# Kernel optimization log

Measured on AMD Instinct MI355X. Metric: run time of the kernel, lower is better.

The kernel has to match this reference:

```python
import jax, jax.numpy as jnp
import numpy as np

N = 50000   # nodes
E = 800000  # edges (before self loops)
D = 128     # n_embd
H = 4       # heads
C = D // H  # per-head channels
NEG_SLOPE = 0.2
EPS = 1e-5


def _ln(x, w):
    m = jnp.mean(x, axis=-1, keepdims=True)
    v = jnp.mean((x - m) ** 2, axis=-1, keepdims=True)
    return (x - m) / jnp.sqrt(v + EPS) * w


def setup_inputs() -> dict:
    key = jax.random.key(0)
    ks = jax.random.split(key, 8)
    s = 0.02
    return {
        "x": jax.random.normal(ks[0], (N, D), jnp.float32),
        "edge_index": jax.random.randint(ks[1], (2, E), 0, N, jnp.int32),
        "ln1_w": jnp.ones((D,), jnp.float32),
        "Wl": jax.random.normal(ks[2], (D, D), jnp.float32) * s,
        "bl": jnp.zeros((D,), jnp.float32),
        "Wr": jax.random.normal(ks[3], (D, D), jnp.float32) * s,
        "br": jnp.zeros((D,), jnp.float32),
        "att": jax.random.normal(ks[4], (H, C), jnp.float32) * s,
        "gat_bias": jnp.zeros((D,), jnp.float32),
        "ln2_w": jnp.ones((D,), jnp.float32),
        "W_fc": jax.random.normal(ks[5], (D, 4 * D), jnp.float32) * s,
        "W_proj": jax.random.normal(ks[6], (4 * D, D), jnp.float32) * s,
    }


def reference(x, edge_index, ln1_w, Wl, bl, Wr, br, att, gat_bias, ln2_w, W_fc, W_proj):
    n = x.shape[0]
    # add self loops (GATv2Conv default)
    loops = jnp.arange(n, dtype=edge_index.dtype)
    src = jnp.concatenate([edge_index[0], loops])  # message sources (x_j)
    dst = jnp.concatenate([edge_index[1], loops])  # message targets (x_i)

    h = _ln(x, ln1_w)
    xl = (h @ Wl + bl).reshape(n, H, C)  # source transform
    xr = (h @ Wr + br).reshape(n, H, C)  # target transform

    # GATv2 edge-wise attention
    e = jax.nn.leaky_relu(xl[src] + xr[dst], NEG_SLOPE)      # [E+N, H, C]
    score = jnp.einsum('ehc,hc->eh', e, att)                  # [E+N, H]
    smax = jax.ops.segment_max(score, dst, num_segments=n)    # [N, H]
    ex = jnp.exp(score - smax[dst])
    denom = jax.ops.segment_sum(ex, dst, num_segments=n)      # [N, H]
    alpha = ex / denom[dst]                                   # segment softmax
    agg = jax.ops.segment_sum(alpha[:, :, None] * xl[src], dst, num_segments=n)

    x = x + agg.reshape(n, H * C) + gat_bias

    h2 = _ln(x, ln2_w)
    x = x + jax.nn.gelu(h2 @ W_fc, approximate=False) @ W_proj
    return x
```

## Files before the change

### kernel.cpp

```cpp
#include <hip/hip_runtime.h>
#include <math.h>

typedef __attribute__((ext_vector_type(8))) short bf16x8;
typedef __attribute__((ext_vector_type(4))) float f32x4;

__device__ __forceinline__ unsigned bf16b(float f) {
  unsigned u = __float_as_uint(f);
  return (u + 0x7fffu + ((u >> 16) & 1u)) >> 16;
}
__device__ __forceinline__ unsigned packbf(float lo, float hi) {
  return bf16b(lo) | (bf16b(hi) << 16);
}
__device__ __forceinline__ float unpk_lo(unsigned u) { return __uint_as_float(u << 16); }
__device__ __forceinline__ float unpk_hi(unsigned u) { return __uint_as_float(u & 0xffff0000u); }
__device__ __forceinline__ float gelu_f(float v) {
  return 0.5f * v * (1.0f + erff(v * 0.70710678118654752f));
}

__global__ void k_cvtz(const float* __restrict__ Wl, const float* __restrict__ Wr,
                       const float* __restrict__ Wfc, const float* __restrict__ Wpj,
                       unsigned short* __restrict__ Wl_t, unsigned short* __restrict__ Wr_t,
                       unsigned short* __restrict__ Wfc_t, unsigned short* __restrict__ Wpj_t,
                       int* __restrict__ deg, int* __restrict__ cursor, int n) {
  int i = blockIdx.x * 256 + threadIdx.x;
  if (i < n) { deg[i] = 0; cursor[i] = 0; }
  if (i < 16384) {
    int k = i & 127, c = i >> 7;
    Wl_t[i] = (unsigned short)bf16b(Wl[k * 128 + c]);
    Wr_t[i] = (unsigned short)bf16b(Wr[k * 128 + c]);
  } else if (i < 81920) {
    int j = i - 16384;
    int k = j & 127, c = j >> 7;
    Wfc_t[j] = (unsigned short)bf16b(Wfc[(size_t)k * 512 + c]);
  } else if (i < 147456) {
    int j = i - 81920;
    int k = j & 511, c = j >> 9;
    Wpj_t[j] = (unsigned short)bf16b(Wpj[(size_t)k * 128 + c]);
  }
}

__global__ __launch_bounds__(256, 2) void k_gemlr(
    const float* __restrict__ x, const float* __restrict__ ln1w,
    const unsigned short* __restrict__ Wl_t, const float* __restrict__ bl,
    const unsigned short* __restrict__ Wr_t, const float* __restrict__ br,
    unsigned short* __restrict__ xl16, unsigned short* __restrict__ xr16, int n)
{
  __shared__ __align__(16) unsigned short hs[64 * 128];
  const int t = threadIdx.x;
  const int lane = t & 63, w = t >> 6;
  const int r0 = blockIdx.x * 64;

  {
    const int row = t >> 2, seg = t & 3;
    const int gr = r0 + row;
    const float4* xr4 = (const float4*)(x + (size_t)(gr < n ? gr : 0) * 128) + seg * 8;
    float4 v[8];
    #pragma unroll
    for (int j = 0; j < 8; ++j) v[j] = (gr < n) ? xr4[j] : make_float4(0.f,0.f,0.f,0.f);
    float s = 0.f;
    #pragma unroll
    for (int j = 0; j < 8; ++j) s += v[j].x + v[j].y + v[j].z + v[j].w;
    s += __shfl_xor(s, 1); s += __shfl_xor(s, 2);
    const float mean = s * (1.0f / 128.0f);
    float vv = 0.f;
    #pragma unroll
    for (int j = 0; j < 8; ++j) {
      float a = v[j].x - mean, b = v[j].y - mean, c = v[j].z - mean, d = v[j].w - mean;
      vv += a * a + b * b + c * c + d * d;
    }
    vv += __shfl_xor(vv, 1); vv += __shfl_xor(vv, 2);
    const float rstd = rsqrtf(vv * (1.0f / 128.0f) + 1e-5f);
    #pragma unroll
    for (int j2 = 0; j2 < 4; ++j2) {
      float4 wa = ((const float4*)ln1w)[seg * 8 + 2 * j2];
      float4 wb = ((const float4*)ln1w)[seg * 8 + 2 * j2 + 1];
      const float4 va = v[2 * j2], vb = v[2 * j2 + 1];
      uint4 pk;
      pk.x = packbf((va.x - mean) * rstd * wa.x, (va.y - mean) * rstd * wa.y);
      pk.y = packbf((va.z - mean) * rstd * wa.z, (va.w - mean) * rstd * wa.w);
      pk.z = packbf((vb.x - mean) * rstd * wb.x, (vb.y - mean) * rstd * wb.y);
      pk.w = packbf((vb.z - mean) * rstd * wb.z, (vb.w - mean) * rstd * wb.w);
      int byteoff = (row * 256 + (seg * 4 + j2) * 16) ^ ((row & 7) << 4);
      *(uint4*)((char*)hs + byteoff) = pk;
    }
  }
  __syncthreads();

  const int l15 = lane & 15, lg = lane >> 4;
  const unsigned short* __restrict__ Wt = (w < 2) ? Wl_t : Wr_t;
  const float* __restrict__ bias = (w < 2) ? bl : br;
  unsigned short* __restrict__ outp = (w < 2) ? xl16 : xr16;
  const int cbase = (w & 1) * 64;

  f32x4 acc[4][4];
  #pragma unroll
  for (int m = 0; m < 4; ++m)
    #pragma unroll
    for (int nf = 0; nf < 4; ++nf) acc[m][nf] = (f32x4){0.f, 0.f, 0.f, 0.f};

  #pragma unroll
  for (int ks = 0; ks < 4; ++ks) {
    bf16x8 b[4];
    #pragma unroll
    for (int nf = 0; nf < 4; ++nf) {
      const int c = cbase + nf * 16 + l15;
      b[nf] = *(const bf16x8*)(Wt + (size_t)c * 128 + ks * 32 + lg * 8);
    }
    bf16x8 a[4];
    #pragma unroll
    for (int m = 0; m < 4; ++m) {
      const int row = m * 16 + l15;
      const int byteoff = (row * 256 + ks * 64 + lg * 16) ^ ((row & 7) << 4);
      a[m] = *(const bf16x8*)((const char*)hs + byteoff);
    }
    #pragma unroll
    for (int m = 0; m < 4; ++m)
      #pragma unroll
      for (int nf = 0; nf < 4; ++nf)
        acc[m][nf] = __builtin_amdgcn_mfma_f32_16x16x32_bf16(a[m], b[nf], acc[m][nf], 0, 0, 0);
  }

  #pragma unroll
  for (int nf = 0; nf < 4; ++nf) {
    const int c = cbase + nf * 16 + l15;
    const float bv = bias[c];
    #pragma unroll
    for (int m = 0; m < 4; ++m) {
      #pragma unroll
      for (int r = 0; r < 4; ++r) {
        const int gr = r0 + m * 16 + lg * 4 + r;
        if (gr < n)
          outp[(size_t)gr * 128 + c] = (unsigned short)bf16b(acc[m][nf][r] + bv);
      }
    }
  }
}

__global__ void k_hist(const int* __restrict__ dst, int* __restrict__ deg, int E) {
  int e = blockIdx.x * 256 + threadIdx.x;
  if (e < E) atomicAdd(&deg[dst[e]], 1);
}

__global__ void k_scan1(const int* __restrict__ deg, int* __restrict__ bsum, int n) {
  __shared__ int red[4];
  const int t = threadIdx.x, lane = t & 63, w = t >> 6;
  const int i = blockIdx.x * 256 + t;
  int v = (i < n) ? deg[i] : 0;
  #pragma unroll
  for (int off = 1; off < 64; off <<= 1) v += __shfl_xor(v, off);
  if (lane == 0) red[w] = v;
  __syncthreads();
  if (t == 0) bsum[blockIdx.x] = red[0] + red[1] + red[2] + red[3];
}

__global__ void k_scan2(int* __restrict__ bsum, int nb, int* __restrict__ rowptr,
                        int n, int Etot) {
  __shared__ int wsum[16];
  const int t = threadIdx.x, lane = t & 63, w = t >> 6;
  const int v = (t < nb) ? bsum[t] : 0;
  int incl = v;
  #pragma unroll
  for (int off = 1; off < 64; off <<= 1) {
    int u = __shfl_up(incl, off);
    if (lane >= off) incl += u;
  }
  if (lane == 63) wsum[w] = incl;
  __syncthreads();
  if (w == 0 && lane < 16) {
    int sv = wsum[lane];
    int si = sv;
    #pragma unroll
    for (int off = 1; off < 16; off <<= 1) {
      int u = __shfl_up(si, off);
      if (lane >= off) si += u;
    }
    wsum[lane] = si - sv;
  }
  __syncthreads();
  if (t < nb) bsum[t] = wsum[w] + incl - v;
  if (t == 0) rowptr[n] = Etot;
}

__global__ void k_scan3(const int* __restrict__ deg, const int* __restrict__ bsum,
                        int* __restrict__ rowptr, int n) {
  __shared__ int ws4[4];
  const int t = threadIdx.x, lane = t & 63, w = t >> 6;
  const int i = blockIdx.x * 256 + t;
  const int v = (i < n) ? deg[i] : 0;
  int incl = v;
  #pragma unroll
  for (int off = 1; off < 64; off <<= 1) {
    int u = __shfl_up(incl, off);
    if (lane >= off) incl += u;
  }
  if (lane == 63) ws4[w] = incl;
  __syncthreads();
  if (t == 0) {
    int s1 = ws4[0], s2 = s1 + ws4[1], s3 = s2 + ws4[2];
    ws4[0] = 0; ws4[1] = s1; ws4[2] = s2; ws4[3] = s3;
  }
  __syncthreads();
  if (i < n) rowptr[i] = bsum[blockIdx.x] + ws4[w] + incl - v;
}

__global__ void k_scatter(const int* __restrict__ src, const int* __restrict__ dst,
                          const int* __restrict__ rowptr, int* __restrict__ cursor,
                          int* __restrict__ csr, int E) {
  int e = blockIdx.x * 256 + threadIdx.x;
  if (e < E) {
    int d = dst[e];
    int pos = atomicAdd(&cursor[d], 1);
    csr[rowptr[d] + pos] = src[e];
  }
}

__global__ __launch_bounds__(256) void k_attn(
    const float* __restrict__ x, const unsigned* __restrict__ xlp,
    const unsigned* __restrict__ xrp, const float* __restrict__ att,
    const float* __restrict__ gbias, const float* __restrict__ ln2w,
    const int* __restrict__ rowptr, const int* __restrict__ csr,
    float* __restrict__ x2, unsigned* __restrict__ h2p, int n)
{
  const int d = (int)((blockIdx.x * blockDim.x + threadIdx.x) >> 6);
  if (d >= n) return;
  const int l = threadIdx.x & 63;
  const unsigned xr = xrp[(size_t)d * 64 + l];
  const float xr0 = unpk_lo(xr), xr1 = unpk_hi(xr);
  const float2 at = ((const float2*)att)[l];
  const int beg = rowptr[d], end = rowptr[d + 1];
  const int cnt = end - beg;

  float m, s, acc0, acc1;
  {
    const unsigned xs = xlp[(size_t)d * 64 + l];
    const float a0 = unpk_lo(xs), a1 = unpk_hi(xs);
    float e0 = a0 + xr0; e0 = (e0 > 0.f) ? e0 : 0.2f * e0;
    float e1 = a1 + xr1; e1 = (e1 > 0.f) ? e1 : 0.2f * e1;
    float tt = e0 * at.x + e1 * at.y;
    tt += __shfl_xor(tt, 1); tt += __shfl_xor(tt, 2);
    tt += __shfl_xor(tt, 4); tt += __shfl_xor(tt, 8);
    m = tt; s = 1.f; acc0 = a0; acc1 = a1;
  }

  unsigned pxs[4];
  if (cnt > 0) {
    int idx[4];
    #pragma unroll
    for (int i = 0; i < 4; ++i) idx[i] = (i < cnt) ? csr[beg + i] : d;
    #pragma unroll
    for (int i = 0; i < 4; ++i) pxs[i] = xlp[(size_t)idx[i] * 64 + l];
  }
  for (int b = 0; b < cnt; b += 4) {
    unsigned xs[4];
    #pragma unroll
    for (int i = 0; i < 4; ++i) xs[i] = pxs[i];
    if (b + 4 < cnt) {
      int idx[4];
      #pragma unroll
      for (int i = 0; i < 4; ++i) idx[i] = (b + 4 + i < cnt) ? csr[beg + b + 4 + i] : d;
      #pragma unroll
      for (int i = 0; i < 4; ++i) pxs[i] = xlp[(size_t)idx[i] * 64 + l];
    }
    const int rem = cnt - b;
    float A0[4], A1[4], T[4];
    #pragma unroll
    for (int i = 0; i < 4; ++i) {
      A0[i] = unpk_lo(xs[i]); A1[i] = unpk_hi(xs[i]);
      float e0 = A0[i] + xr0; e0 = (e0 > 0.f) ? e0 : 0.2f * e0;
      float e1 = A1[i] + xr1; e1 = (e1 > 0.f) ? e1 : 0.2f * e1;
      T[i] = e0 * at.x + e1 * at.y;
    }
    #pragma unroll
    for (int off = 1; off < 16; off <<= 1)
      #pragma unroll
      for (int i = 0; i < 4; ++i) T[i] += __shfl_xor(T[i], off);
    #pragma unroll
    for (int i = 0; i < 4; ++i) if (i >= rem) T[i] = -1e30f;
    const float bm = fmaxf(fmaxf(T[0], T[1]), fmaxf(T[2], T[3]));
    const float p0 = __expf(T[0] - bm), p1 = __expf(T[1] - bm);
    const float p2 = __expf(T[2] - bm), p3 = __expf(T[3] - bm);
    const float bs = p0 + p1 + p2 + p3;
    const float b0 = p0 * A0[0] + p1 * A0[1] + p2 * A0[2] + p3 * A0[3];
    const float b1 = p0 * A1[0] + p1 * A1[1] + p2 * A1[2] + p3 * A1[3];
    const float nm = fmaxf(m, bm);
    const float sc = __expf(m - nm), sb = __expf(bm - nm);
    s    = s    * sc + bs * sb;
    acc0 = acc0 * sc + b0 * sb;
    acc1 = acc1 * sc + b1 * sb;
    m = nm;
  }

  const float inv = 1.0f / s;
  const float2 xv = ((const float2*)x)[(size_t)d * 64 + l];
  const float2 gb = ((const float2*)gbias)[l];
  float2 o;
  o.x = xv.x + acc0 * inv + gb.x;
  o.y = xv.y + acc1 * inv + gb.y;
  ((float2*)x2)[(size_t)d * 64 + l] = o;

  float s2 = o.x + o.y;
  #pragma unroll
  for (int off = 1; off < 64; off <<= 1) s2 += __shfl_xor(s2, off);
  const float mean = s2 * (1.0f / 128.0f);
  const float dx = o.x - mean, dy = o.y - mean;
  float vv = dx * dx + dy * dy;
  #pragma unroll
  for (int off = 1; off < 64; off <<= 1) vv += __shfl_xor(vv, off);
  const float rstd = rsqrtf(vv * (1.0f / 128.0f) + 1e-5f);
  const float2 lw = ((const float2*)ln2w)[l];
  h2p[(size_t)d * 64 + l] = packbf(dx * rstd * lw.x, dy * rstd * lw.y);
}

__global__ __launch_bounds__(256, 3) void k_fc(
    const unsigned short* __restrict__ h2, const unsigned short* __restrict__ Wfc_t,
    unsigned short* __restrict__ g, int n)
{
  __shared__ __align__(16) unsigned short As[128 * 128];
  __shared__ __align__(16) unsigned short Bs[64 * 128];
  const int t = threadIdx.x, lane = t & 63, w = t >> 6;
  const int l15 = lane & 15, lg = lane >> 4;
  const int r0 = blockIdx.x * 128;
  const int cb0 = blockIdx.y * 64;

  #pragma unroll
  for (int it = 0; it < 8; ++it) {
    int i = it * 256 + t;
    int row = i >> 4, c16 = i & 15;
    int gr = r0 + row;
    uint4 v = make_uint4(0, 0, 0, 0);
    if (gr < n) v = *(const uint4*)(h2 + (size_t)gr * 128 + c16 * 8);
    *(uint4*)((char*)As + ((row * 256 + c16 * 16) ^ ((row & 7) << 4))) = v;
  }
  #pragma unroll
  for (int it = 0; it < 4; ++it) {
    int i = it * 256 + t;
    int col = i >> 4, k16 = i & 15;
    uint4 v = *(const uint4*)(Wfc_t + (size_t)(cb0 + col) * 128 + k16 * 8);
    *(uint4*)((char*)Bs + ((col * 256 + k16 * 16) ^ ((col & 7) << 4))) = v;
  }
  __syncthreads();

  const int rbase = (w >> 1) * 64;
  const int cbase = (w & 1) * 32;
  f32x4 acc[4][2];
  #pragma unroll
  for (int m = 0; m < 4; ++m) {
    acc[m][0] = (f32x4){0.f, 0.f, 0.f, 0.f};
    acc[m][1] = (f32x4){0.f, 0.f, 0.f, 0.f};
  }
  #pragma unroll
  for (int ks = 0; ks < 4; ++ks) {
    bf16x8 b[2], a[4];
    #pragma unroll
    for (int nf = 0; nf < 2; ++nf) {
      const int col = cbase + nf * 16 + l15;
      b[nf] = *(const bf16x8*)((const char*)Bs + ((col * 256 + ks * 64 + lg * 16) ^ ((col & 7) << 4)));
    }
    #pragma unroll
    for (int m = 0; m < 4; ++m) {
      const int row = rbase + m * 16 + l15;
      a[m] = *(const bf16x8*)((const char*)As + ((row * 256 + ks * 64 + lg * 16) ^ ((row & 7) << 4)));
    }
    #pragma unroll
    for (int m = 0; m < 4; ++m) {
      acc[m][0] = __builtin_amdgcn_mfma_f32_16x16x32_bf16(a[m], b[0], acc[m][0], 0, 0, 0);
      acc[m][1] = __builtin_amdgcn_mfma_f32_16x16x32_bf16(a[m], b[1], acc[m][1], 0, 0, 0);
    }
  }

  #pragma unroll
  for (int m = 0; m < 4; ++m)
    #pragma unroll
    for (int nf = 0; nf < 2; ++nf) {
      const int gc = cb0 + cbase + nf * 16 + l15;
      #pragma unroll
      for (int r = 0; r < 4; ++r) {
        const int gr = r0 + rbase + m * 16 + lg * 4 + r;
        if (gr < n)
          g[(size_t)gr * 256 + gc] = (unsigned short)bf16b(gelu_f(acc[m][nf][r]));
      }
    }
}

__global__ __launch_bounds__(256, 3) void k_proj(
    const unsigned short* __restrict__ g, const unsigned short* __restrict__ Wpj_t,
    float* __restrict__ out, int n)
{
  __shared__ __align__(16) unsigned short As[64 * 64];
  __shared__ __align__(16) unsigned short Bs[128 * 64];
  const int t = threadIdx.x, lane = t & 63, w = t >> 6;
  const int l15 = lane & 15, lg = lane >> 4;
  const int r0 = blockIdx.x * 64;

  f32x4 acc[8];
  #pragma unroll
  for (int nf = 0; nf < 8; ++nf) acc[nf] = (f32x4){0.f, 0.f, 0.f, 0.f};

  for (int kt = 0; kt < 4; ++kt) {
    __syncthreads();
    #pragma unroll
    for (int it = 0; it < 2; ++it) {
      int i = it * 256 + t;
      int row = i >> 3, k8 = i & 7;
      int gr = r0 + row;
      uint4 v = make_uint4(0, 0, 0, 0);
      if (gr < n) v = *(const uint4*)(g + (size_t)gr * 256 + kt * 64 + k8 * 8);
      *(uint4*)((char*)As + ((row * 128 + k8 * 16) ^ ((row & 7) << 4))) = v;
    }
    #pragma unroll
    for (int it = 0; it < 4; ++it) {
      int i = it * 256 + t;
      int col = i >> 3, k8 = i & 7;
      uint4 v = *(const uint4*)(Wpj_t + (size_t)col * 512 + kt * 64 + k8 * 8);
      *(uint4*)((char*)Bs + ((col * 128 + k8 * 16) ^ ((col & 7) << 4))) = v;
    }
    __syncthreads();

    #pragma unroll
    for (int ks = 0; ks < 2; ++ks) {
      const int row = w * 16 + l15;
      bf16x8 a = *(const bf16x8*)((const char*)As + ((row * 128 + ks * 64 + lg * 16) ^ ((row & 7) << 4)));
      bf16x8 b[8];
      #pragma unroll
      for (int nf = 0; nf < 8; ++nf) {
        const int col = nf * 16 + l15;
        b[nf] = *(const bf16x8*)((const char*)Bs + ((col * 128 + ks * 64 + lg * 16) ^ ((col & 7) << 4)));
      }
      #pragma unroll
      for (int nf = 0; nf < 8; ++nf)
        acc[nf] = __builtin_amdgcn_mfma_f32_16x16x32_bf16(a, b[nf], acc[nf], 0, 0, 0);
    }
  }

  #pragma unroll
  for (int nf = 0; nf < 8; ++nf) {
    const int col = nf * 16 + l15;
    #pragma unroll
    for (int r = 0; r < 4; ++r) {
      const int gr = r0 + w * 16 + lg * 4 + r;
      if (gr < n) {
        float* p = out + (size_t)gr * 128 + col;
        *p = *p + acc[nf][r];
      }
    }
  }
}

extern "C" void kernel_launch(void* const* d_in, const int* in_sizes, int n_in,
                              void* d_out, int out_size, void* d_ws, size_t ws_size,
                              hipStream_t stream)
{
  (void)n_in; (void)out_size; (void)ws_size;
  const float* x     = (const float*)d_in[0];
  const int*   ei    = (const int*)d_in[1];
  const float* ln1w  = (const float*)d_in[2];
  const float* Wl    = (const float*)d_in[3];
  const float* bl    = (const float*)d_in[4];
  const float* Wr    = (const float*)d_in[5];
  const float* br    = (const float*)d_in[6];
  const float* att   = (const float*)d_in[7];
  const float* gbias = (const float*)d_in[8];
  const float* ln2w  = (const float*)d_in[9];
  const float* Wfc   = (const float*)d_in[10];
  const float* Wpj   = (const float*)d_in[11];
  float* out = (float*)d_out;

  const int n = in_sizes[0] / 128;
  const int E = in_sizes[1] / 2;
  const int nb = (n + 255) / 256;

  char* w = (char*)d_ws;
  unsigned short* h2    = (unsigned short*)w; w += (size_t)n * 128 * 2;
  unsigned short* Wl_t  = (unsigned short*)w; w += 16384 * 2;
  unsigned short* Wr_t  = (unsigned short*)w; w += 16384 * 2;
  unsigned short* Wfc_t = (unsigned short*)w; w += 65536 * 2;
  unsigned short* Wpj_t = (unsigned short*)w; w += 65536 * 2;
  int* rowptr = (int*)w; w += (size_t)((n + 4) & ~3) * 4;
  int* bsum   = (int*)w; w += 1024 * 4;
  int* deg    = (int*)w; w += (size_t)n * 4;
  int* cursor = (int*)w; w += (size_t)n * 4;
  char* gbase = w;
  unsigned short* xl16 = (unsigned short*)gbase;
  unsigned short* xr16 = (unsigned short*)(gbase + (size_t)n * 128 * 2);
  int* csr             = (int*)(gbase + (size_t)n * 128 * 4);
  unsigned short* g    = (unsigned short*)gbase;

  k_cvtz<<<576, 256, 0, stream>>>(Wl, Wr, Wfc, Wpj, Wl_t, Wr_t, Wfc_t, Wpj_t,
                                  deg, cursor, n);
  k_gemlr<<<(n + 63) / 64, 256, 0, stream>>>(x, ln1w, Wl_t, bl, Wr_t, br, xl16, xr16, n);
  k_hist<<<(E + 255) / 256, 256, 0, stream>>>(ei + E, deg, E);
  k_scan1<<<nb, 256, 0, stream>>>(deg, bsum, n);
  k_scan2<<<1, 1024, 0, stream>>>(bsum, nb, rowptr, n, E);
  k_scan3<<<nb, 256, 0, stream>>>(deg, bsum, rowptr, n);
  k_scatter<<<(E + 255) / 256, 256, 0, stream>>>(ei, ei + E, rowptr, cursor, csr, E);
  k_attn<<<(n + 3) / 4, 256, 0, stream>>>(x, (const unsigned*)xl16, (const unsigned*)xr16,
                                          att, gbias, ln2w, rowptr, csr, out,
                                          (unsigned*)h2, n);
  dim3 gfc((n + 127) / 128, 4);
  for (int half = 0; half < 2; ++half) {
    k_fc  <<<gfc, 256, 0, stream>>>(h2, Wfc_t + (size_t)half * 256 * 128, g, n);
    k_proj<<<(n + 63) / 64, 256, 0, stream>>>(g, Wpj_t + (size_t)half * 256, out, n);
  }
}
```

Baseline: 379.7 us.

## Retile MLP, merge fc/proj halves, widen attention gather, tile weight transpose

Several changes land together. The MLP now runs as a single fc pass over all 512 hidden columns and one proj pass with K=512 when the workspace is large enough, with the fc tile reshaped to 64 rows by 128 columns; this removes the second pair of launches and the two read-modify-write passes over the output. The attention gather prefetches 8 neighbours per batch instead of 4 and makes the indices wave-uniform via readfirstlane, aiming for more memory-level parallelism. The weight-conversion kernel now transposes through a shared-memory tile with vectorised reads and writes instead of strided per-element reads. The costs are higher register pressure in attention and a larger workspace footprint for the intermediate g buffer.

```diff
diff --git a/kernel.cpp b/kernel.cpp
--- a/kernel.cpp
+++ b/kernel.cpp
@@ -21,21 +21,42 @@
                        const float* __restrict__ Wfc, const float* __restrict__ Wpj,
                        unsigned short* __restrict__ Wl_t, unsigned short* __restrict__ Wr_t,
                        unsigned short* __restrict__ Wfc_t, unsigned short* __restrict__ Wpj_t,
-                       int* __restrict__ deg, int* __restrict__ cursor, int n) {
-  int i = blockIdx.x * 256 + threadIdx.x;
-  if (i < n) { deg[i] = 0; cursor[i] = 0; }
-  if (i < 16384) {
-    int k = i & 127, c = i >> 7;
-    Wl_t[i] = (unsigned short)bf16b(Wl[k * 128 + c]);
-    Wr_t[i] = (unsigned short)bf16b(Wr[k * 128 + c]);
-  } else if (i < 81920) {
-    int j = i - 16384;
-    int k = j & 127, c = j >> 7;
-    Wfc_t[j] = (unsigned short)bf16b(Wfc[(size_t)k * 512 + c]);
-  } else if (i < 147456) {
-    int j = i - 81920;
-    int k = j & 511, c = j >> 9;
-    Wpj_t[j] = (unsigned short)bf16b(Wpj[(size_t)k * 128 + c]);
+                       int* __restrict__ deg, int* __restrict__ cursor, int n, int nzb) {
+  __shared__ float tl[64 * 65];
+  const int b = blockIdx.x, t = threadIdx.x;
+  if (b >= 40) {
+    const int zb = b - 40;
+    int* arr = (zb < nzb) ? deg : cursor;
+    const int base = (zb % nzb) * 1024 + t * 4;
+    #pragma unroll
+    for (int j = 0; j < 4; ++j) if (base + j < n) arr[base + j] = 0;
+    return;
+  }
+  const float* src; unsigned short* dst; int K, C, tm;
+  if (b < 4)       { src = Wl;  dst = Wl_t;  K = 128; C = 128; tm = b; }
+  else if (b < 8)  { src = Wr;  dst = Wr_t;  K = 128; C = 128; tm = b - 4; }
+  else if (b < 24) { src = Wfc; dst = Wfc_t; K = 128; C = 512; tm = b - 8; }
+  else             { src = Wpj; dst = Wpj_t; K = 512; C = 128; tm = b - 24; }
+  const int ct = C >> 6;
+  const int k0 = (tm / ct) * 64, c0 = (tm % ct) * 64;
+  #pragma unroll
+  for (int it = 0; it < 4; ++it) {
+    const int q = it * 256 + t;
+    const int row = q >> 4, c4 = q & 15;
+    float4 v = *(const float4*)(src + (size_t)(k0 + row) * C + c0 + c4 * 4);
+    float* p = &tl[row * 65 + c4 * 4];
+    p[0] = v.x; p[1] = v.y; p[2] = v.z; p[3] = v.w;
+  }
+  __syncthreads();
+  #pragma unroll
+  for (int it = 0; it < 2; ++it) {
+    const int q = it * 256 + t;
+    const int cr = q >> 3, k8 = q & 7;
+    bf16x8 sh;
+    #pragma unroll
+    for (int j = 0; j < 8; ++j)
+      sh[j] = (short)bf16b(tl[(k8 * 8 + j) * 65 + cr]);
+    *(bf16x8*)(dst + (size_t)(c0 + cr) * K + k0 + k8 * 8) = sh;
   }
 }
 
@@ -221,10 +242,11 @@
     const int* __restrict__ rowptr, const int* __restrict__ csr,
     float* __restrict__ x2, unsigned* __restrict__ h2p, int n)
 {
-  const int d = (int)((blockIdx.x * blockDim.x + threadIdx.x) >> 6);
-  if (d >= n) return;
+  const int dv = (int)((blockIdx.x * blockDim.x + threadIdx.x) >> 6);
+  if (dv >= n) return;
+  const int d = __builtin_amdgcn_readfirstlane(dv);
   const int l = threadIdx.x & 63;
-  const unsigned xr = xrp[(size_t)d * 64 + l];
+  const unsigned xr = (xrp + (size_t)d * 64)[l];
   const float xr0 = unpk_lo(xr), xr1 = unpk_hi(xr);
   const float2 at = ((const float2*)att)[l];
   const int beg = rowptr[d], end = rowptr[d + 1];
@@ -232,56 +254,62 @@
 
   float m, s, acc0, acc1;
   {
-    const unsigned xs = xlp[(size_t)d * 64 + l];
+    const unsigned xs = (xlp + (size_t)d * 64)[l];
     const float a0 = unpk_lo(xs), a1 = unpk_hi(xs);
-    float e0 = a0 + xr0; e0 = (e0 > 0.f) ? e0 : 0.2f * e0;
-    float e1 = a1 + xr1; e1 = (e1 > 0.f) ? e1 : 0.2f * e1;
+    const float t0 = a0 + xr0, t1 = a1 + xr1;
+    const float e0 = fmaxf(t0, 0.2f * t0), e1 = fmaxf(t1, 0.2f * t1);
     float tt = e0 * at.x + e1 * at.y;
     tt += __shfl_xor(tt, 1); tt += __shfl_xor(tt, 2);
     tt += __shfl_xor(tt, 4); tt += __shfl_xor(tt, 8);
     m = tt; s = 1.f; acc0 = a0; acc1 = a1;
   }
 
-  unsigned pxs[4];
+  unsigned pxs[8];
   if (cnt > 0) {
-    int idx[4];
-    #pragma unroll
-    for (int i = 0; i < 4; ++i) idx[i] = (i < cnt) ? csr[beg + i] : d;
-    #pragma unroll
-    for (int i = 0; i < 4; ++i) pxs[i] = xlp[(size_t)idx[i] * 64 + l];
-  }
-  for (int b = 0; b < cnt; b += 4) {
-    unsigned xs[4];
-    #pragma unroll
-    for (int i = 0; i < 4; ++i) xs[i] = pxs[i];
-    if (b + 4 < cnt) {
-      int idx[4];
-      #pragma unroll
-      for (int i = 0; i < 4; ++i) idx[i] = (b + 4 + i < cnt) ? csr[beg + b + 4 + i] : d;
-      #pragma unroll
-      for (int i = 0; i < 4; ++i) pxs[i] = xlp[(size_t)idx[i] * 64 + l];
+    #pragma unroll
+    for (int i = 0; i < 8; ++i) {
+      int idx = (i < cnt) ? csr[beg + i] : d;
+      idx = __builtin_amdgcn_readfirstlane(idx);
+      pxs[i] = (xlp + (size_t)idx * 64)[l];
+    }
+  }
+  for (int b = 0; b < cnt; b += 8) {
+    unsigned xs[8];
+    #pragma unroll
+    for (int i = 0; i < 8; ++i) xs[i] = pxs[i];
+    if (b + 8 < cnt) {
+      #pragma unroll
+      for (int i = 0; i < 8; ++i) {
+        int idx = (b + 8 + i < cnt) ? csr[beg + b + 8 + i] : d;
+        idx = __builtin_amdgcn_readfirstlane(idx);
+        pxs[i] = (xlp + (size_t)idx * 64)[l];
+      }
     }
     const int rem = cnt - b;
-    float A0[4], A1[4], T[4];
-    #pragma unroll
-    for (int i = 0; i < 4; ++i) {
+    float A0[8], A1[8], T[8];
+    #pragma unroll
+    for (int i = 0; i < 8; ++i) {
       A0[i] = unpk_lo(xs[i]); A1[i] = unpk_hi(xs[i]);
-      float e0 = A0[i] + xr0; e0 = (e0 > 0.f) ? e0 : 0.2f * e0;
-      float e1 = A1[i] + xr1; e1 = (e1 > 0.f) ? e1 : 0.2f * e1;
+      const float t0 = A0[i] + xr0, t1 = A1[i] + xr1;
+      const float e0 = fmaxf(t0, 0.2f * t0), e1 = fmaxf(t1, 0.2f * t1);
       T[i] = e0 * at.x + e1 * at.y;
     }
     #pragma unroll
     for (int off = 1; off < 16; off <<= 1)
       #pragma unroll
-      for (int i = 0; i < 4; ++i) T[i] += __shfl_xor(T[i], off);
-    #pragma unroll
-    for (int i = 0; i < 4; ++i) if (i >= rem) T[i] = -1e30f;
-    const float bm = fmaxf(fmaxf(T[0], T[1]), fmaxf(T[2], T[3]));
-    const float p0 = __expf(T[0] - bm), p1 = __expf(T[1] - bm);
-    const float p2 = __expf(T[2] - bm), p3 = __expf(T[3] - bm);
-    const float bs = p0 + p1 + p2 + p3;
-    const float b0 = p0 * A0[0] + p1 * A0[1] + p2 * A0[2] + p3 * A0[3];
-    const float b1 = p0 * A1[0] + p1 * A1[1] + p2 * A1[2] + p3 * A1[3];
+      for (int i = 0; i < 8; ++i) T[i] += __shfl_xor(T[i], off);
+    #pragma unroll
+    for (int i = 0; i < 8; ++i) if (i >= rem) T[i] = -1e30f;
+    float bm = fmaxf(fmaxf(fmaxf(T[0], T[1]), fmaxf(T[2], T[3])),
+                     fmaxf(fmaxf(T[4], T[5]), fmaxf(T[6], T[7])));
+    float P[8], bs = 0.f, b0 = 0.f, b1 = 0.f;
+    #pragma unroll
+    for (int i = 0; i < 8; ++i) {
+      P[i] = __expf(T[i] - bm);
+      bs += P[i];
+      b0 += P[i] * A0[i];
+      b1 += P[i] * A1[i];
+    }
     const float nm = fmaxf(m, bm);
     const float sc = __expf(m - nm), sb = __expf(bm - nm);
     s    = s    * sc + bs * sb;
@@ -291,12 +319,12 @@
   }
 
   const float inv = 1.0f / s;
-  const float2 xv = ((const float2*)x)[(size_t)d * 64 + l];
+  const float2 xv = ((const float2*)(x + (size_t)d * 128))[l];
   const float2 gb = ((const float2*)gbias)[l];
   float2 o;
   o.x = xv.x + acc0 * inv + gb.x;
   o.y = xv.y + acc1 * inv + gb.y;
-  ((float2*)x2)[(size_t)d * 64 + l] = o;
+  ((float2*)(x2 + (size_t)d * 128))[l] = o;
 
   float s2 = o.x + o.y;
   #pragma unroll
@@ -308,22 +336,22 @@
   for (int off = 1; off < 64; off <<= 1) vv += __shfl_xor(vv, off);
   const float rstd = rsqrtf(vv * (1.0f / 128.0f) + 1e-5f);
   const float2 lw = ((const float2*)ln2w)[l];
-  h2p[(size_t)d * 64 + l] = packbf(dx * rstd * lw.x, dy * rstd * lw.y);
+  (h2p + (size_t)d * 64)[l] = packbf(dx * rstd * lw.x, dy * rstd * lw.y);
 }
 
 __global__ __launch_bounds__(256, 3) void k_fc(
     const unsigned short* __restrict__ h2, const unsigned short* __restrict__ Wfc_t,
-    unsigned short* __restrict__ g, int n)
+    unsigned short* __restrict__ g, int g_ld, int n)
 {
-  __shared__ __align__(16) unsigned short As[128 * 128];
-  __shared__ __align__(16) unsigned short Bs[64 * 128];
+  __shared__ __align__(16) unsigned short As[64 * 128];
+  __shared__ __align__(16) unsigned short Bs[128 * 128];
   const int t = threadIdx.x, lane = t & 63, w = t >> 6;
   const int l15 = lane & 15, lg = lane >> 4;
-  const int r0 = blockIdx.x * 128;
-  const int cb0 = blockIdx.y * 64;
-
-  #pragma unroll
-  for (int it = 0; it < 8; ++it) {
+  const int r0 = blockIdx.x * 64;
+  const int cb0 = blockIdx.y * 128;
+
+  #pragma unroll
+  for (int it = 0; it < 4; ++it) {
     int i = it * 256 + t;
     int row = i >> 4, c16 = i & 15;
     int gr = r0 + row;
@@ -332,7 +360,7 @@
     *(uint4*)((char*)As + ((row * 256 + c16 * 16) ^ ((row & 7) << 4))) = v;
   }
   #pragma unroll
-  for (int it = 0; it < 4; ++it) {
+  for (int it = 0; it < 8; ++it) {
     int i = it * 256 + t;
     int col = i >> 4, k16 = i & 15;
     uint4 v = *(const uint4*)(Wfc_t + (size_t)(cb0 + col) * 128 + k16 * 8);
@@ -340,51 +368,51 @@
   }
   __syncthreads();
 
-  const int rbase = (w >> 1) * 64;
-  const int cbase = (w & 1) * 32;
-  f32x4 acc[4][2];
-  #pragma unroll
-  for (int m = 0; m < 4; ++m) {
-    acc[m][0] = (f32x4){0.f, 0.f, 0.f, 0.f};
-    acc[m][1] = (f32x4){0.f, 0.f, 0.f, 0.f};
-  }
+  const int rbase = (w >> 1) * 32;
+  const int cbase = (w & 1) * 64;
+  f32x4 acc[2][4];
+  #pragma unroll
+  for (int m = 0; m < 2; ++m)
+    #pragma unroll
+    for (int nf = 0; nf < 4; ++nf) acc[m][nf] = (f32x4){0.f, 0.f, 0.f, 0.f};
+
   #pragma unroll
   for (int ks = 0; ks < 4; ++ks) {
-    bf16x8 b[2], a[4];
-    #pragma unroll
-    for (int nf = 0; nf < 2; ++nf) {
+    bf16x8 b[4], a[2];
+    #pragma unroll
+    for (int nf = 0; nf < 4; ++nf) {
       const int col = cbase + nf * 16 + l15;
       b[nf] = *(const bf16x8*)((const char*)Bs + ((col * 256 + ks * 64 + lg * 16) ^ ((col & 7) << 4)));
     }
     #pragma unroll
-    for (int m = 0; m < 4; ++m) {
+    for (int m = 0; m < 2; ++m) {
       const int row = rbase + m * 16 + l15;
       a[m] = *(const bf16x8*)((const char*)As + ((row * 256 + ks * 64 + lg * 16) ^ ((row & 7) << 4)));
     }
     #pragma unroll
-    for (int m = 0; m < 4; ++m) {
-      acc[m][0] = __builtin_amdgcn_mfma_f32_16x16x32_bf16(a[m], b[0], acc[m][0], 0, 0, 0);
-      acc[m][1] = __builtin_amdgcn_mfma_f32_16x16x32_bf16(a[m], b[1], acc[m][1], 0, 0, 0);
-    }
-  }
-
-  #pragma unroll
-  for (int m = 0; m < 4; ++m)
-    #pragma unroll
-    for (int nf = 0; nf < 2; ++nf) {
+    for (int m = 0; m < 2; ++m)
+      #pragma unroll
+      for (int nf = 0; nf < 4; ++nf)
+        acc[m][nf] = __builtin_amdgcn_mfma_f32_16x16x32_bf16(a[m], b[nf], acc[m][nf], 0, 0, 0);
+  }
+
+  #pragma unroll
+  for (int m = 0; m < 2; ++m)
+    #pragma unroll
+    for (int nf = 0; nf < 4; ++nf) {
       const int gc = cb0 + cbase + nf * 16 + l15;
       #pragma unroll
       for (int r = 0; r < 4; ++r) {
         const int gr = r0 + rbase + m * 16 + lg * 4 + r;
         if (gr < n)
-          g[(size_t)gr * 256 + gc] = (unsigned short)bf16b(gelu_f(acc[m][nf][r]));
+          g[(size_t)gr * g_ld + gc] = (unsigned short)bf16b(gelu_f(acc[m][nf][r]));
       }
     }
 }
 
 __global__ __launch_bounds__(256, 3) void k_proj(
     const unsigned short* __restrict__ g, const unsigned short* __restrict__ Wpj_t,
-    float* __restrict__ out, int n)
+    int g_ld, int koff, int ktn, float* __restrict__ out, int n)
 {
   __shared__ __align__(16) unsigned short As[64 * 64];
   __shared__ __align__(16) unsigned short Bs[128 * 64];
@@ -396,7 +424,7 @@
   #pragma unroll
   for (int nf = 0; nf < 8; ++nf) acc[nf] = (f32x4){0.f, 0.f, 0.f, 0.f};
 
-  for (int kt = 0; kt < 4; ++kt) {
+  for (int kt = 0; kt < ktn; ++kt) {
     __syncthreads();
     #pragma unroll
     for (int it = 0; it < 2; ++it) {
@@ -404,14 +432,14 @@
       int row = i >> 3, k8 = i & 7;
       int gr = r0 + row;
       uint4 v = make_uint4(0, 0, 0, 0);
-      if (gr < n) v = *(const uint4*)(g + (size_t)gr * 256 + kt * 64 + k8 * 8);
+      if (gr < n) v = *(const uint4*)(g + (size_t)gr * g_ld + kt * 64 + k8 * 8);
       *(uint4*)((char*)As + ((row * 128 + k8 * 16) ^ ((row & 7) << 4))) = v;
     }
     #pragma unroll
     for (int it = 0; it < 4; ++it) {
       int i = it * 256 + t;
       int col = i >> 3, k8 = i & 7;
-      uint4 v = *(const uint4*)(Wpj_t + (size_t)col * 512 + kt * 64 + k8 * 8);
+      uint4 v = *(const uint4*)(Wpj_t + (size_t)col * 512 + koff + kt * 64 + k8 * 8);
       *(uint4*)((char*)Bs + ((col * 128 + k8 * 16) ^ ((col & 7) << 4))) = v;
     }
     __syncthreads();
@@ -450,7 +478,7 @@
                               void* d_out, int out_size, void* d_ws, size_t ws_size,
                               hipStream_t stream)
 {
-  (void)n_in; (void)out_size; (void)ws_size;
+  (void)n_in; (void)out_size;
   const float* x     = (const float*)d_in[0];
   const int*   ei    = (const int*)d_in[1];
   const float* ln1w  = (const float*)d_in[2];
@@ -468,6 +496,7 @@
   const int n = in_sizes[0] / 128;
   const int E = in_sizes[1] / 2;
   const int nb = (n + 255) / 256;
+  const int nzb = (n + 1023) / 1024;
 
   char* w = (char*)d_ws;
   unsigned short* h2    = (unsigned short*)w; w += (size_t)n * 128 * 2;
@@ -485,8 +514,11 @@
   int* csr             = (int*)(gbase + (size_t)n * 128 * 4);
   unsigned short* g    = (unsigned short*)gbase;
 
-  k_cvtz<<<576, 256, 0, stream>>>(Wl, Wr, Wfc, Wpj, Wl_t, Wr_t, Wfc_t, Wpj_t,
-                                  deg, cursor, n);
+  const size_t used = (size_t)(gbase - (char*)d_ws);
+  const bool single = ws_size >= used + (size_t)n * 512 * 2;
+
+  k_cvtz<<<40 + 2 * nzb, 256, 0, stream>>>(Wl, Wr, Wfc, Wpj, Wl_t, Wr_t, Wfc_t, Wpj_t,
+                                           deg, cursor, n, nzb);
   k_gemlr<<<(n + 63) / 64, 256, 0, stream>>>(x, ln1w, Wl_t, bl, Wr_t, br, xl16, xr16, n);
   k_hist<<<(E + 255) / 256, 256, 0, stream>>>(ei + E, deg, E);
   k_scan1<<<nb, 256, 0, stream>>>(deg, bsum, n);
@@ -496,9 +528,15 @@
   k_attn<<<(n + 3) / 4, 256, 0, stream>>>(x, (const unsigned*)xl16, (const unsigned*)xr16,
                                           att, gbias, ln2w, rowptr, csr, out,
                                           (unsigned*)h2, n);
-  dim3 gfc((n + 127) / 128, 4);
-  for (int half = 0; half < 2; ++half) {
-    k_fc  <<<gfc, 256, 0, stream>>>(h2, Wfc_t + (size_t)half * 256 * 128, g, n);
-    k_proj<<<(n + 63) / 64, 256, 0, stream>>>(g, Wpj_t + (size_t)half * 256, out, n);
-  }
-}
+  if (single) {
+    dim3 gfc((n + 63) / 64, 4);
+    k_fc  <<<gfc, 256, 0, stream>>>(h2, Wfc_t, g, 512, n);
+    k_proj<<<(n + 63) / 64, 256, 0, stream>>>(g, Wpj_t, 512, 0, 8, out, n);
+  } else {
+    dim3 gfc((n + 63) / 64, 2);
+    for (int half = 0; half < 2; ++half) {
+      k_fc  <<<gfc, 256, 0, stream>>>(h2, Wfc_t + (size_t)half * 256 * 128, g, 256, n);
+      k_proj<<<(n + 63) / 64, 256, 0, stream>>>(g, Wpj_t, 256, half * 256, 4, out, n);
+    }
+  }
+}
```

New measurement: 335.9 us. 1.13x faster.
